# Performance work log

Hardware: AMD Instinct MI355X
Metric: run time of the kernel (lower is better)

The kernel has to match this reference:

```python
import jax, jax.numpy as jnp
import numpy as np

N = 20000       # nodes
E = 320000      # edges
IN_C = 256      # in_channels
HID = 256       # hidden_channels
H = 8           # heads
D = HID // H    # head dim = 32
SCALE = 1.0 / np.sqrt(D)
DIN = IN_C + HID


def _lin_params(key, din, dout):
    k1, k2 = jax.random.split(key)
    W = jax.random.normal(k1, (din, dout), jnp.float32) * (1.0 / np.sqrt(din))
    b = jax.random.normal(k2, (dout,), jnp.float32) * 0.01
    return W, b


def setup_inputs() -> dict:
    key = jax.random.key(0)
    ks = jax.random.split(key, 16)
    inp = {
        "x": jax.random.normal(ks[0], (N, IN_C), jnp.float32),
        "h": jax.random.normal(ks[1], (N, HID), jnp.float32) * 0.1,
        "edge_index": jax.random.randint(ks[2], (2, E), 0, N, dtype=jnp.int32),
    }
    i = 3
    for name in ["z", "r", "c"]:
        for p in ["Wq", "Wk", "Wv", "Ws"]:
            W, b = _lin_params(ks[i], DIN, HID)
            i += 1
            inp[f"{name}_{p}"] = W
            inp[f"{name}_b{p[1].lower()}"] = b
    return inp


def _tconv(x, src, dst, Wq, bq, Wk, bk, Wv, bv, Ws, bs):
    """PyG TransformerConv (eval mode, concat=True, root_weight=True, beta=False)."""
    # dense per-node projections, then edge-indexed gathers
    q = (x @ Wq + bq)[dst].reshape(-1, H, D)   # [E, H, D] query at target
    k = (x @ Wk + bk)[src].reshape(-1, H, D)   # [E, H, D] key at source
    v = (x @ Wv + bv)[src].reshape(-1, H, D)   # [E, H, D] value at source
    logits = jnp.sum(q * k, axis=-1) * SCALE   # [E, H]
    # segment softmax over each destination's neighborhood
    m = jax.ops.segment_max(logits, dst, num_segments=N)
    e = jnp.exp(logits - m[dst])
    s = jax.ops.segment_sum(e, dst, num_segments=N)
    alpha = e / (s[dst] + 1e-16)               # [E, H]
    agg = jax.ops.segment_sum(alpha[:, :, None] * v, dst, num_segments=N)
    return agg.reshape(N, HID) + x @ Ws + bs   # attention out + root skip


def reference(x, h, edge_index,
              z_Wq, z_bq, z_Wk, z_bk, z_Wv, z_bv, z_Ws, z_bs,
              r_Wq, r_bq, r_Wk, r_bk, r_Wv, r_bv, r_Ws, r_bs,
              c_Wq, c_bq, c_Wk, c_bk, c_Wv, c_bv, c_Ws, c_bs):
    src, dst = edge_index[0], edge_index[1]
    h_in = jnp.concatenate([x, h], axis=-1)                      # [N, DIN]
    z = jax.nn.sigmoid(_tconv(h_in, src, dst, z_Wq, z_bq, z_Wk, z_bk, z_Wv, z_bv, z_Ws, z_bs))
    r = jax.nn.sigmoid(_tconv(h_in, src, dst, r_Wq, r_bq, r_Wk, r_bk, r_Wv, r_bv, r_Ws, r_bs))
    h_cand = jnp.concatenate([x, r * h], axis=-1)                # [N, DIN]
    h_tilde = jnp.tanh(_tconv(h_cand, src, dst, c_Wq, c_bq, c_Wk, c_bk, c_Wv, c_bv, c_Ws, c_bs))
    return z * h + (1.0 - z) * h_tilde
```

## Files before the change

### kernel.cpp

```cpp
#include <hip/hip_runtime.h>
#include <hip/hip_bf16.h>
#include <math.h>

#define NNODES 20000
#define MPAD 20096
#define NEDGES 320000
#define HIDC 256
#define DINC 512
#define NHEAD 8
#define HDIM 32
#define SCALE 0.17677669529663687f

typedef __attribute__((ext_vector_type(8))) short short8;
typedef __attribute__((ext_vector_type(4))) short svec4;
typedef __attribute__((ext_vector_type(4))) float f32x4;

__device__ __forceinline__ void gload_lds16(const void* g, void* l) {
    __builtin_amdgcn_global_load_lds(
        (const __attribute__((address_space(1))) unsigned int*)g,
        (__attribute__((address_space(3))) unsigned int*)l, 16, 0, 0);
}

__device__ __forceinline__ float bfbits(unsigned short u) {
    return __uint_as_float(((unsigned)u) << 16);
}

__global__ __launch_bounds__(256) void concat_xh(const float* __restrict__ x,
                                                 const float* __restrict__ h,
                                                 __hip_bfloat16* __restrict__ out) {
    int i = blockIdx.x * 256 + threadIdx.x;
    int total = MPAD * DINC;
    if (i >= total) return;
    int row = i >> 9;
    int col = i & 511;
    float v = 0.f;
    if (row < NNODES)
        v = (col < HIDC) ? x[row * HIDC + col] : h[row * HIDC + (col - HIDC)];
    out[i] = __float2bfloat16(v);
}

struct WPtrs { const float* p[12]; };

__global__ __launch_bounds__(256) void transpose_w(WPtrs wp, __hip_bfloat16* __restrict__ out) {
    __shared__ float t[64][65];
    int mat = blockIdx.z;
    int kt = blockIdx.x * 64;
    int nt = blockIdx.y * 64;
    const float* W = wp.p[mat];
    int c = threadIdx.x & 63, r4 = threadIdx.x >> 6;
#pragma unroll
    for (int rr = 0; rr < 16; ++rr) {
        int k_l = r4 + rr * 4;
        t[k_l][c] = W[(kt + k_l) * HIDC + nt + c];
    }
    __syncthreads();
#pragma unroll
    for (int rr = 0; rr < 16; ++rr) {
        int n_l = r4 + rr * 4;
        out[mat * (HIDC * DINC) + (nt + n_l) * DINC + kt + c] =
            __float2bfloat16(t[c][n_l]);
    }
}

__global__ __launch_bounds__(256) void count_deg(const int* __restrict__ dst,
                                                 int* __restrict__ deg) {
    int e = blockIdx.x * 256 + threadIdx.x;
    if (e >= NEDGES) return;
    atomicAdd(&deg[dst[e]], 1);
}

__global__ __launch_bounds__(1024) void exscan(const int* __restrict__ deg,
                                               int* __restrict__ rowptr,
                                               int* __restrict__ pos) {
    __shared__ int sdata[1024];
    __shared__ int s_carry;
    const int tid = threadIdx.x;
    if (tid == 0) { s_carry = 0; rowptr[0] = 0; }
    __syncthreads();
    for (int base = 0; base < NNODES; base += 1024) {
        int i = base + tid;
        int v = (i < NNODES) ? deg[i] : 0;
        sdata[tid] = v;
        __syncthreads();
        for (int off = 1; off < 1024; off <<= 1) {
            int t = (tid >= off) ? sdata[tid - off] : 0;
            __syncthreads();
            sdata[tid] += t;
            __syncthreads();
        }
        int incl = sdata[tid];
        int carry = s_carry;
        if (i < NNODES) {
            int ex = carry + incl - v;
            rowptr[i] = ex;
            pos[i] = ex;
            if (i == NNODES - 1) rowptr[NNODES] = carry + incl;
        }
        __syncthreads();
        if (tid == 1023) s_carry = carry + incl;
        __syncthreads();
    }
}

__global__ __launch_bounds__(256) void scatter_src(const int* __restrict__ src,
                                                   const int* __restrict__ dst,
                                                   int* __restrict__ pos,
                                                   int* __restrict__ csrc) {
    int e = blockIdx.x * 256 + threadIdx.x;
    if (e >= NEDGES) return;
    int idx = atomicAdd(&pos[dst[e]], 1);
    csrc[idx] = src[e];
}

struct GemmArgs { const float* bias[8]; void* C[8]; int ldc[8]; unsigned bf16mask; };

template <int NZ>
__global__ __launch_bounds__(256) void gemm_mfma(
    const __hip_bfloat16* __restrict__ A,
    const __hip_bfloat16* __restrict__ WtBase,
    GemmArgs ga) {
    __shared__ __align__(16) char smem[2][32768];

    int nwg = gridDim.x;
    int per = nwg >> 3;
    int lin = (blockIdx.x & 7) * per + (blockIdx.x >> 3);
    int bmIdx = lin / NZ;
    int nz = lin % NZ;
    int bm = bmIdx * 128;
    int bn = (nz & 1) * 128;
    int z = nz >> 1;

    const __hip_bfloat16* Bt = WtBase + (size_t)z * (HIDC * DINC);
    const float* bias = ga.bias[z];
    void* Cv = ga.C[z];
    int ldc = ga.ldc[z];
    bool isb = (ga.bf16mask >> z) & 1;

    int tid = threadIdx.x;
    int wave = tid >> 6, lane = tid & 63;
    int lrow = lane >> 3;
    int lcol = (lane & 7) ^ lrow;

    int wr = wave >> 1, wc = wave & 1;
    int m_base = wr * 64, n_base = wc * 64;
    int l16 = lane & 15, lk = lane >> 4;

    f32x4 acc[4][4] = {};

    auto stage = [&](int buf, int kt) {
        char* As = smem[buf];
        char* Bs = smem[buf] + 16384;
#pragma unroll
        for (int c4 = 0; c4 < 4; ++c4) {
            int c = wave * 4 + c4;
            gload_lds16(&A[(size_t)(bm + c * 8 + lrow) * DINC + kt + lcol * 8],
                        As + c * 1024);
        }
#pragma unroll
        for (int c4 = 0; c4 < 4; ++c4) {
            int c = wave * 4 + c4;
            gload_lds16(&Bt[(size_t)(bn + c * 8 + lrow) * DINC + kt + lcol * 8],
                        Bs + c * 1024);
        }
    };

    auto compute = [&](int buf) {
        char* As = smem[buf];
        char* Bs = smem[buf] + 16384;
#pragma unroll
        for (int kk = 0; kk < 2; ++kk) {
            short8 af[4], bf[4];
#pragma unroll
            for (int f = 0; f < 4; ++f) {
                int row = m_base + f * 16 + l16;
                int lin2 = row * 128 + (kk * 32 + lk * 8) * 2;
                af[f] = *(const short8*)(As + (lin2 ^ ((row & 7) << 4)));
                int rowb = n_base + f * 16 + l16;
                int linb = rowb * 128 + (kk * 32 + lk * 8) * 2;
                bf[f] = *(const short8*)(Bs + (linb ^ ((rowb & 7) << 4)));
            }
#pragma unroll
            for (int i = 0; i < 4; ++i)
#pragma unroll
                for (int j = 0; j < 4; ++j)
                    acc[i][j] = __builtin_amdgcn_mfma_f32_16x16x32_bf16(
                        af[i], bf[j], acc[i][j], 0, 0, 0);
        }
    };

    stage(0, 0);
#pragma unroll
    for (int t = 0; t < 8; ++t) {
        int cur = t & 1;
        if (t < 7) {
            stage(cur ^ 1, (t + 1) * 64);
            asm volatile("s_waitcnt vmcnt(8)" ::: "memory");
        } else {
            asm volatile("s_waitcnt vmcnt(0)" ::: "memory");
        }
        __builtin_amdgcn_s_barrier();
        __builtin_amdgcn_sched_barrier(0);
        compute(cur);
        __builtin_amdgcn_sched_barrier(0);
        __builtin_amdgcn_s_barrier();
    }

#pragma unroll
    for (int i = 0; i < 4; ++i) {
#pragma unroll
        for (int j = 0; j < 4; ++j) {
            int n = bn + n_base + j * 16 + l16;
            float bia = bias[n];
#pragma unroll
            for (int r = 0; r < 4; ++r) {
                int m = bm + m_base + i * 16 + lk * 4 + r;
                if (m < NNODES) {
                    float val = acc[i][j][r] + bia;
                    if (isb)
                        ((__hip_bfloat16*)Cv)[(size_t)m * ldc + n] = __float2bfloat16(val);
                    else
                        ((float*)Cv)[(size_t)m * ldc + n] = val;
                }
            }
        }
    }
}

__global__ __launch_bounds__(256) void attn_zr(
    const __hip_bfloat16* __restrict__ Qz, const __hip_bfloat16* __restrict__ Qr,
    const __hip_bfloat16* __restrict__ K2, const __hip_bfloat16* __restrict__ V2,
    const float* __restrict__ Sz, const float* __restrict__ Sr,
    const int* __restrict__ rowptr, const int* __restrict__ csrc,
    const float* __restrict__ h,
    float* __restrict__ Zout, __hip_bfloat16* __restrict__ abuf) {
    int lane = threadIdx.x & 63;
    int node = blockIdx.x * 4 + (threadIdx.x >> 6);

    int eA = lane >> 4;
    int gA = (lane >> 3) & 1;
    int hA = lane & 7;
    int gC = lane >> 5;
    int cL = lane & 31;
    int cBase = cL * 8;
    int hC = cL >> 2;
    int wsrc = gC * 8 + hC;
    size_t kOff = (size_t)gA * 256 + hA * 32;
    size_t vOff = (size_t)gC * 256 + cBase;

    const __hip_bfloat16* Qa = gA ? Qr : Qz;
    short8 qs[4];
    {
        const short8* Qrow = (const short8*)&Qa[(size_t)node * HIDC + hA * 32];
        qs[0] = Qrow[0]; qs[1] = Qrow[1]; qs[2] = Qrow[2]; qs[3] = Qrow[3];
    }

    int beg = rowptr[node], end = rowptr[node + 1];
    float acc[8] = {};
    float s_priv = 0.f;

    auto issueKV = [&](int snL, short8* k, short8* v) {
        int mySn = __shfl(snL, eA);
        const short8* Kp = (const short8*)&K2[(size_t)mySn * 512 + kOff];
        k[0] = Kp[0]; k[1] = Kp[1]; k[2] = Kp[2]; k[3] = Kp[3];
#pragma unroll
        for (int e = 0; e < 4; ++e) {
            int sne = __shfl(snL, e);
            v[e] = *(const short8*)&V2[(size_t)sne * 512 + vOff];
        }
    };
    auto computeC = [&](int snL, int cnt, short8* k, short8* v) {
        float w = 0.f;
        if (eA < cnt) {
            float dot = 0.f;
#pragma unroll
            for (int i = 0; i < 4; ++i) {
                short8 kv = k[i], qv = qs[i];
#pragma unroll
                for (int j = 0; j < 8; ++j)
                    dot += bfbits((unsigned short)qv[j]) * bfbits((unsigned short)kv[j]);
            }
            w = __expf(dot * SCALE);
        }
#pragma unroll
        for (int e = 0; e < 4; ++e) {
            float we = __shfl(w, e * 16 + wsrc);
            if (e < cnt) {
                short8 vv = v[e];
#pragma unroll
                for (int j = 0; j < 8; ++j) acc[j] += we * bfbits((unsigned short)vv[j]);
                s_priv += we;
            }
        }
    };

    if (beg < end) {
        short8 kA[4], vA[4], kB[4], vB[4];
        int baseA = beg;
        int cntA = min(4, end - baseA);
        int snLA = (lane < cntA) ? csrc[baseA + lane] : 0;
        issueKV(snLA, kA, vA);
        int baseB = baseA + 4, cntB = 0, snLB = 0;
        if (baseB < end) { cntB = min(4, end - baseB); snLB = (lane < cntB) ? csrc[baseB + lane] : 0; }
        for (;;) {
            if (baseB < end) issueKV(snLB, kB, vB);
            int baseN = baseB + 4, cntN = 0, snLN = 0;
            if (baseN < end) { cntN = min(4, end - baseN); snLN = (lane < cntN) ? csrc[baseN + lane] : 0; }
            computeC(snLA, cntA, kA, vA);
            if (baseB >= end) break;
            if (baseN < end) issueKV(snLN, kA, vA);
            int baseN2 = baseN + 4, cntN2 = 0, snLN2 = 0;
            if (baseN2 < end) { cntN2 = min(4, end - baseN2); snLN2 = (lane < cntN2) ? csrc[baseN2 + lane] : 0; }
            computeC(snLB, cntB, kB, vB);
            if (baseN >= end) break;
            baseA = baseN; cntA = cntN; snLA = snLN;
            baseB = baseN2; cntB = cntN2; snLB = snLN2;
        }
    }

    float inv = 1.f / (s_priv + 1e-16f);
    const float* Sx = gC ? Sr : Sz;
    float g[8];
#pragma unroll
    for (int j = 0; j < 8; ++j) {
        float p = acc[j] * inv + Sx[(size_t)node * HIDC + cBase + j];
        g[j] = 1.f / (1.f + __expf(-p));
    }
    if (gC == 0) {
        float* Zp = &Zout[(size_t)node * HIDC + cBase];
#pragma unroll
        for (int j = 0; j < 8; ++j) Zp[j] = g[j];
    } else {
        const float* hp = &h[(size_t)node * HIDC + cBase];
        __hip_bfloat16* ap = &abuf[(size_t)node * DINC + HIDC + cBase];
#pragma unroll
        for (int j = 0; j < 8; ++j) ap[j] = __float2bfloat16(g[j] * hp[j]);
    }
}

__global__ __launch_bounds__(256) void attn_c(
    const __hip_bfloat16* __restrict__ Q, const __hip_bfloat16* __restrict__ K,
    const __hip_bfloat16* __restrict__ V, const float* __restrict__ S,
    const int* __restrict__ rowptr, const int* __restrict__ csrc,
    const float* __restrict__ zbuf, const float* __restrict__ h,
    float* __restrict__ out) {
    int lane = threadIdx.x & 63;
    int node = blockIdx.x * 4 + (threadIdx.x >> 6);

    int eA = lane >> 3;
    int hA = lane & 7;
    int cBase = lane * 4;
    int hC = lane >> 3;

    short8 qs[4];
    {
        const short8* Qrow = (const short8*)&Q[(size_t)node * HIDC + hA * 32];
        qs[0] = Qrow[0]; qs[1] = Qrow[1]; qs[2] = Qrow[2]; qs[3] = Qrow[3];
    }

    int beg = rowptr[node], end = rowptr[node + 1];
    float acc[4] = {};
    float s_priv = 0.f;

    auto issueKV = [&](int snL, short8* k, svec4* v) {
        int mySn = __shfl(snL, eA);
        const short8* Kp = (const short8*)&K[(size_t)mySn * HIDC + hA * 32];
        k[0] = Kp[0]; k[1] = Kp[1]; k[2] = Kp[2]; k[3] = Kp[3];
#pragma unroll
        for (int e = 0; e < 8; ++e) {
            int sne = __shfl(snL, e);
            v[e] = *(const svec4*)&V[(size_t)sne * HIDC + cBase];
        }
    };
    auto computeC = [&](int snL, int cnt, short8* k, svec4* v) {
        float w = 0.f;
        if (eA < cnt) {
            float dot = 0.f;
#pragma unroll
            for (int i = 0; i < 4; ++i) {
                short8 kv = k[i], qv = qs[i];
#pragma unroll
                for (int j = 0; j < 8; ++j)
                    dot += bfbits((unsigned short)qv[j]) * bfbits((unsigned short)kv[j]);
            }
            w = __expf(dot * SCALE);
        }
#pragma unroll
        for (int e = 0; e < 8; ++e) {
            float we = __shfl(w, e * 8 + hC);
            if (e < cnt) {
                svec4 vv = v[e];
#pragma unroll
                for (int j = 0; j < 4; ++j) acc[j] += we * bfbits((unsigned short)vv[j]);
                s_priv += we;
            }
        }
    };

    if (beg < end) {
        short8 kA[4], kB[4];
        svec4 vA[8], vB[8];
        int baseA = beg;
        int cntA = min(8, end - baseA);
        int snLA = (lane < cntA) ? csrc[baseA + lane] : 0;
        issueKV(snLA, kA, vA);
        int baseB = baseA + 8, cntB = 0, snLB = 0;
        if (baseB < end) { cntB = min(8, end - baseB); snLB = (lane < cntB) ? csrc[baseB + lane] : 0; }
        for (;;) {
            if (baseB < end) issueKV(snLB, kB, vB);
            int baseN = baseB + 8, cntN = 0, snLN = 0;
            if (baseN < end) { cntN = min(8, end - baseN); snLN = (lane < cntN) ? csrc[baseN + lane] : 0; }
            computeC(snLA, cntA, kA, vA);
            if (baseB >= end) break;
            if (baseN < end) issueKV(snLN, kA, vA);
            int baseN2 = baseN + 8, cntN2 = 0, snLN2 = 0;
            if (baseN2 < end) { cntN2 = min(8, end - baseN2); snLN2 = (lane < cntN2) ? csrc[baseN2 + lane] : 0; }
            computeC(snLB, cntB, kB, vB);
            if (baseN >= end) break;
            baseA = baseN; cntA = cntN; snLA = snLN;
            baseB = baseN2; cntB = cntN2; snLB = snLN2;
        }
    }

    float inv = 1.f / (s_priv + 1e-16f);
    f32x4 o;
#pragma unroll
    for (int j = 0; j < 4; ++j) {
        float pre = acc[j] * inv + S[(size_t)node * HIDC + cBase + j];
        float ht = tanhf(pre);
        float zz = zbuf[(size_t)node * HIDC + cBase + j];
        float hh = h[(size_t)node * HIDC + cBase + j];
        o[j] = zz * hh + (1.f - zz) * ht;
    }
    *(f32x4*)&out[(size_t)node * HIDC + cBase] = o;
}

extern "C" void kernel_launch(void* const* d_in, const int* in_sizes, int n_in,
                              void* d_out, int out_size, void* d_ws, size_t ws_size,
                              hipStream_t stream) {
    const float* x = (const float*)d_in[0];
    const float* h = (const float*)d_in[1];
    const int* ei = (const int*)d_in[2];
    const float* Wf[3][4];
    const float* B[3][4];
    for (int g = 0; g < 3; ++g)
        for (int p = 0; p < 4; ++p) {
            Wf[g][p] = (const float*)d_in[3 + g * 8 + p * 2];
            B[g][p] = (const float*)d_in[3 + g * 8 + p * 2 + 1];
        }

    char* ws = (char*)d_ws;
    size_t off = 0;
    auto alloc = [&](size_t bytes) {
        void* p = ws + off;
        off = (off + bytes + 255) & ~(size_t)255;
        return p;
    };
    __hip_bfloat16* Abuf = (__hip_bfloat16*)alloc((size_t)MPAD * DINC * 2);
    __hip_bfloat16* Wt = (__hip_bfloat16*)alloc((size_t)12 * HIDC * DINC * 2);
    __hip_bfloat16* Qz = (__hip_bfloat16*)alloc((size_t)NNODES * HIDC * 2);
    __hip_bfloat16* Qr = (__hip_bfloat16*)alloc((size_t)NNODES * HIDC * 2);
    __hip_bfloat16* K2 = (__hip_bfloat16*)alloc((size_t)NNODES * 512 * 2);
    __hip_bfloat16* V2 = (__hip_bfloat16*)alloc((size_t)NNODES * 512 * 2);
    float* Sz = (float*)alloc((size_t)NNODES * HIDC * 4);
    float* Sr = (float*)alloc((size_t)NNODES * HIDC * 4);
    float* Zb = (float*)alloc((size_t)NNODES * HIDC * 4);
    int* deg = (int*)alloc((size_t)NNODES * 4);
    int* rowptr = (int*)alloc((size_t)(NNODES + 1) * 4);
    int* pos = (int*)alloc((size_t)NNODES * 4);
    int* csrc = (int*)alloc((size_t)NEDGES * 4);

    const int* srcArr = ei;
    const int* dstArr = ei + NEDGES;

    WPtrs wp;
    for (int g = 0; g < 3; ++g)
        for (int p = 0; p < 4; ++p) wp.p[g * 4 + p] = Wf[g][p];

    (void)hipMemsetAsync(deg, 0, NNODES * sizeof(int), stream);
    concat_xh<<<(MPAD * DINC + 255) / 256, 256, 0, stream>>>(x, h, Abuf);
    transpose_w<<<dim3(8, 4, 12), 256, 0, stream>>>(wp, Wt);
    count_deg<<<(NEDGES + 255) / 256, 256, 0, stream>>>(dstArr, deg);
    exscan<<<1, 1024, 0, stream>>>(deg, rowptr, pos);
    scatter_src<<<(NEDGES + 255) / 256, 256, 0, stream>>>(srcArr, dstArr, pos, csrc);

    {
        GemmArgs ga;
        for (int p = 0; p < 4; ++p) { ga.bias[p] = B[0][p]; ga.bias[4 + p] = B[1][p]; }
        ga.C[0] = Qz;        ga.ldc[0] = 256;
        ga.C[1] = K2;        ga.ldc[1] = 512;
        ga.C[2] = V2;        ga.ldc[2] = 512;
        ga.C[3] = Sz;        ga.ldc[3] = 256;
        ga.C[4] = Qr;        ga.ldc[4] = 256;
        ga.C[5] = K2 + 256;  ga.ldc[5] = 512;
        ga.C[6] = V2 + 256;  ga.ldc[6] = 512;
        ga.C[7] = Sr;        ga.ldc[7] = 256;
        ga.bf16mask = 0x77;
        gemm_mfma<16><<<(MPAD / 128) * 16, 256, 0, stream>>>(Abuf, Wt, ga);
    }
    attn_zr<<<NNODES / 4, 256, 0, stream>>>(Qz, Qr, K2, V2, Sz, Sr,
                                            rowptr, csrc, h, Zb, Abuf);
    {
        GemmArgs ga;
        for (int p = 0; p < 8; ++p) { ga.bias[p] = B[2][p & 3]; ga.C[p] = nullptr; ga.ldc[p] = 256; }
        ga.C[0] = Qz; ga.C[1] = K2; ga.C[2] = V2; ga.C[3] = Sz;
        ga.bf16mask = 0x7;
        gemm_mfma<8><<<(MPAD / 128) * 8, 256, 0, stream>>>(
            Abuf, Wt + (size_t)8 * HIDC * DINC, ga);
    }
    attn_c<<<NNODES / 4, 256, 0, stream>>>(Qz, K2, V2, Sz, rowptr, csrc,
                                           Zb, h, (float*)d_out);
}
```

Before: 400.4 us.

## Store skip projections in bf16 and single-buffer the GEMM LDS pipeline

The root-skip projection outputs (Sz, Sr, S) are now written in bf16 instead of fp32, and the attention kernels read them with vectorized loads. This halves the bytes written by the GEMMs and read by the attention epilogues, at some cost in precision. The GEMM also drops its double-buffered LDS pipeline for a single 32KB buffer with two __syncthreads per k-tile. That frees LDS, which may raise occupancy, but global loads no longer overlap with MFMA compute.

```diff
diff --git a/kernel.cpp b/kernel.cpp
--- a/kernel.cpp
+++ b/kernel.cpp
@@ -119,7 +119,7 @@
     const __hip_bfloat16* __restrict__ A,
     const __hip_bfloat16* __restrict__ WtBase,
     GemmArgs ga) {
-    __shared__ __align__(16) char smem[2][32768];
+    __shared__ __align__(16) char smem[32768];
 
     int nwg = gridDim.x;
     int per = nwg >> 3;
@@ -145,11 +145,12 @@
     int m_base = wr * 64, n_base = wc * 64;
     int l16 = lane & 15, lk = lane >> 4;
 
+    char* As = smem;
+    char* Bs = smem + 16384;
+
     f32x4 acc[4][4] = {};
 
-    auto stage = [&](int buf, int kt) {
-        char* As = smem[buf];
-        char* Bs = smem[buf] + 16384;
+    for (int kt = 0; kt < DINC; kt += 64) {
 #pragma unroll
         for (int c4 = 0; c4 < 4; ++c4) {
             int c = wave * 4 + c4;
@@ -162,11 +163,7 @@
             gload_lds16(&Bt[(size_t)(bn + c * 8 + lrow) * DINC + kt + lcol * 8],
                         Bs + c * 1024);
         }
-    };
-
-    auto compute = [&](int buf) {
-        char* As = smem[buf];
-        char* Bs = smem[buf] + 16384;
+        __syncthreads();
 #pragma unroll
         for (int kk = 0; kk < 2; ++kk) {
             short8 af[4], bf[4];
@@ -186,23 +183,7 @@
                     acc[i][j] = __builtin_amdgcn_mfma_f32_16x16x32_bf16(
                         af[i], bf[j], acc[i][j], 0, 0, 0);
         }
-    };
-
-    stage(0, 0);
-#pragma unroll
-    for (int t = 0; t < 8; ++t) {
-        int cur = t & 1;
-        if (t < 7) {
-            stage(cur ^ 1, (t + 1) * 64);
-            asm volatile("s_waitcnt vmcnt(8)" ::: "memory");
-        } else {
-            asm volatile("s_waitcnt vmcnt(0)" ::: "memory");
-        }
-        __builtin_amdgcn_s_barrier();
-        __builtin_amdgcn_sched_barrier(0);
-        compute(cur);
-        __builtin_amdgcn_sched_barrier(0);
-        __builtin_amdgcn_s_barrier();
+        __syncthreads();
     }
 
 #pragma unroll
@@ -229,7 +210,7 @@
 __global__ __launch_bounds__(256) void attn_zr(
     const __hip_bfloat16* __restrict__ Qz, const __hip_bfloat16* __restrict__ Qr,
     const __hip_bfloat16* __restrict__ K2, const __hip_bfloat16* __restrict__ V2,
-    const float* __restrict__ Sz, const float* __restrict__ Sr,
+    const __hip_bfloat16* __restrict__ Sz, const __hip_bfloat16* __restrict__ Sr,
     const int* __restrict__ rowptr, const int* __restrict__ csrc,
     const float* __restrict__ h,
     float* __restrict__ Zout, __hip_bfloat16* __restrict__ abuf) {
@@ -318,11 +299,12 @@
     }
 
     float inv = 1.f / (s_priv + 1e-16f);
-    const float* Sx = gC ? Sr : Sz;
+    const __hip_bfloat16* Sx = gC ? Sr : Sz;
+    short8 sv = *(const short8*)&Sx[(size_t)node * HIDC + cBase];
     float g[8];
 #pragma unroll
     for (int j = 0; j < 8; ++j) {
-        float p = acc[j] * inv + Sx[(size_t)node * HIDC + cBase + j];
+        float p = acc[j] * inv + bfbits((unsigned short)sv[j]);
         g[j] = 1.f / (1.f + __expf(-p));
     }
     if (gC == 0) {
@@ -339,7 +321,7 @@
 
 __global__ __launch_bounds__(256) void attn_c(
     const __hip_bfloat16* __restrict__ Q, const __hip_bfloat16* __restrict__ K,
-    const __hip_bfloat16* __restrict__ V, const float* __restrict__ S,
+    const __hip_bfloat16* __restrict__ V, const __hip_bfloat16* __restrict__ S,
     const int* __restrict__ rowptr, const int* __restrict__ csrc,
     const float* __restrict__ zbuf, const float* __restrict__ h,
     float* __restrict__ out) {
@@ -422,10 +404,11 @@
     }
 
     float inv = 1.f / (s_priv + 1e-16f);
+    svec4 sv = *(const svec4*)&S[(size_t)node * HIDC + cBase];
     f32x4 o;
 #pragma unroll
     for (int j = 0; j < 4; ++j) {
-        float pre = acc[j] * inv + S[(size_t)node * HIDC + cBase + j];
+        float pre = acc[j] * inv + bfbits((unsigned short)sv[j]);
         float ht = tanhf(pre);
         float zz = zbuf[(size_t)node * HIDC + cBase + j];
         float hh = h[(size_t)node * HIDC + cBase + j];
@@ -461,8 +444,8 @@
     __hip_bfloat16* Qr = (__hip_bfloat16*)alloc((size_t)NNODES * HIDC * 2);
     __hip_bfloat16* K2 = (__hip_bfloat16*)alloc((size_t)NNODES * 512 * 2);
     __hip_bfloat16* V2 = (__hip_bfloat16*)alloc((size_t)NNODES * 512 * 2);
-    float* Sz = (float*)alloc((size_t)NNODES * HIDC * 4);
-    float* Sr = (float*)alloc((size_t)NNODES * HIDC * 4);
+    __hip_bfloat16* Sz = (__hip_bfloat16*)alloc((size_t)NNODES * HIDC * 2);
+    __hip_bfloat16* Sr = (__hip_bfloat16*)alloc((size_t)NNODES * HIDC * 2);
     float* Zb = (float*)alloc((size_t)NNODES * HIDC * 4);
     int* deg = (int*)alloc((size_t)NNODES * 4);
     int* rowptr = (int*)alloc((size_t)(NNODES + 1) * 4);
@@ -494,7 +477,7 @@
         ga.C[5] = K2 + 256;  ga.ldc[5] = 512;
         ga.C[6] = V2 + 256;  ga.ldc[6] = 512;
         ga.C[7] = Sr;        ga.ldc[7] = 256;
-        ga.bf16mask = 0x77;
+        ga.bf16mask = 0xFF;
         gemm_mfma<16><<<(MPAD / 128) * 16, 256, 0, stream>>>(Abuf, Wt, ga);
     }
     attn_zr<<<NNODES / 4, 256, 0, stream>>>(Qz, Qr, K2, V2, Sz, Sr,
@@ -503,7 +486,7 @@
         GemmArgs ga;
         for (int p = 0; p < 8; ++p) { ga.bias[p] = B[2][p & 3]; ga.C[p] = nullptr; ga.ldc[p] = 256; }
         ga.C[0] = Qz; ga.C[1] = K2; ga.C[2] = V2; ga.C[3] = Sz;
-        ga.bf16mask = 0x7;
+        ga.bf16mask = 0xFF;
         gemm_mfma<8><<<(MPAD / 128) * 8, 256, 0, stream>>>(
             Abuf, Wt + (size_t)8 * HIDC * DINC, ga);
     }
```

After: 403.7 us. Within noise of the previous version (+0.8%).
